# Optimization experiments

Hardware: AMD Instinct MI355X
Metric: run time of the kernel (lower is better)

Reference implementation:

```python
import jax, jax.numpy as jnp
import numpy as np

H = 128            # hidden_size; also the chunk length from torch.split(x, hidden_size)
NUM_CHUNKS = 4096  # B
INPUT_SIZE = 1
NUM_CLASSES = 1


def setup_inputs() -> dict:
    key = jax.random.key(0)
    ks = jax.random.split(key, 7)
    N = NUM_CHUNKS * H
    s = 1.0 / np.sqrt(H).astype(np.float32)
    x = jax.random.normal(ks[0], (N,), dtype=jnp.float32)
    W_ih = jax.random.uniform(ks[1], (4 * H, INPUT_SIZE), minval=-s, maxval=s, dtype=jnp.float32)
    W_hh = jax.random.uniform(ks[2], (4 * H, H), minval=-s, maxval=s, dtype=jnp.float32)
    b_ih = jax.random.uniform(ks[3], (4 * H,), minval=-s, maxval=s, dtype=jnp.float32)
    b_hh = jax.random.uniform(ks[4], (4 * H,), minval=-s, maxval=s, dtype=jnp.float32)
    fc_W = jax.random.uniform(ks[5], (NUM_CLASSES, H), minval=-s, maxval=s, dtype=jnp.float32)
    fc_b = jax.random.uniform(ks[6], (NUM_CLASSES,), minval=-s, maxval=s, dtype=jnp.float32)
    return {"x": x, "W_ih": W_ih, "W_hh": W_hh, "b_ih": b_ih, "b_hh": b_hh,
            "fc_W": fc_W, "fc_b": fc_b}


def reference(x, W_ih, W_hh, b_ih, b_hh, fc_W, fc_b):
    # Original: split flat x into chunks of length H, run each chunk as a
    # batch-1 LSTM (input_size=1), take final hidden state, apply fc_out.
    # Here all chunks are batched into one fused recurrent pass.
    Hh = W_hh.shape[1]
    xb = x.reshape(-1, Hh, 1)                                  # [B, T=H, 1]
    # input projection is time-parallel: precompute gate pre-activations
    pre = jnp.einsum('bti,gi->btg', xb, W_ih) + b_ih + b_hh    # [B, T, 4H]

    def step(carry, p_t):
        h, c = carry                                           # [B, H] each
        gates = p_t + h @ W_hh.T                               # [B, 4H]
        i, f, g, o = jnp.split(gates, 4, axis=-1)              # PyTorch gate order i,f,g,o
        i = jax.nn.sigmoid(i)
        f = jax.nn.sigmoid(f)
        g = jnp.tanh(g)
        o = jax.nn.sigmoid(o)
        c = f * c + i * g
        h = o * jnp.tanh(c)
        return (h, c), None

    B = xb.shape[0]
    h0 = jnp.zeros((B, Hh), dtype=x.dtype)
    c0 = jnp.zeros((B, Hh), dtype=x.dtype)
    (hT, _), _ = jax.lax.scan(step, (h0, c0), jnp.swapaxes(pre, 0, 1))
    return hT @ fc_W.T + fc_b                                  # [B, num_classes]
```

## Files before the change

### kernel.cpp

```cpp
#include <hip/hip_runtime.h>


#define H   128
#define T   128
#define MB  16
#define BLOCK 512
#define HSTRIDE 136

typedef _Float16 f16x8 __attribute__((ext_vector_type(8)));
typedef float    f32x4 __attribute__((ext_vector_type(4)));

__device__ __forceinline__ float fsig(float v) {
    float e = __expf(-v);
    return __builtin_amdgcn_rcpf(1.0f + e);
}
__device__ __forceinline__ float ftanh(float v) {
    float e = __expf(2.0f * v);
    return 1.0f - 2.0f * __builtin_amdgcn_rcpf(1.0f + e);
}

__launch_bounds__(BLOCK, 2)
__global__ void lstm_fused_kernel(const float* __restrict__ x,
                                  const float* __restrict__ W_ih,
                                  const float* __restrict__ W_hh,
                                  const float* __restrict__ b_ih,
                                  const float* __restrict__ b_hh,
                                  const float* __restrict__ fc_W,
                                  const float* __restrict__ fc_b,
                                  float* __restrict__ out)
{
    __shared__ float xs[MB][T];
    __shared__ __align__(16) _Float16 hbuf[2][MB][HSTRIDE];

    const int tid  = threadIdx.x;
    const int wave = tid >> 6;
    const int lane = tid & 63;
    const int l15  = lane & 15;
    const int q    = lane >> 4;
    const int jcol = wave * 16 + l15;

    {
        const float4* src = (const float4*)(x + (size_t)blockIdx.x * (MB * T));
        float4* dst = (float4*)(&xs[0][0]);
        dst[tid] = src[tid];
    }
    for (int i = tid; i < MB * HSTRIDE; i += BLOCK)
        (&hbuf[0][0][0])[i] = (_Float16)0.0f;

    f16x8 wf[4][4];
    float wih[4], bias[4];
    #pragma unroll
    for (int g = 0; g < 4; ++g) {
        const int n = g * H + jcol;
        wih[g]  = W_ih[n];
        bias[g] = b_ih[n] + b_hh[n];
        #pragma unroll
        for (int kc = 0; kc < 4; ++kc) {
            const float* wp = W_hh + (size_t)n * H + kc * 32 + q * 8;
            float4 w0 = ((const float4*)wp)[0];
            float4 w1 = ((const float4*)wp)[1];
            f16x8 f;
            f[0] = (_Float16)w0.x; f[1] = (_Float16)w0.y;
            f[2] = (_Float16)w0.z; f[3] = (_Float16)w0.w;
            f[4] = (_Float16)w1.x; f[5] = (_Float16)w1.y;
            f[6] = (_Float16)w1.z; f[7] = (_Float16)w1.w;
            wf[g][kc] = f;
        }
    }

    float c[4] = {0.f, 0.f, 0.f, 0.f};

    __syncthreads();

    for (int t = 0; t < T; ++t) {
        const int rb = t & 1;
        const int wb = rb ^ 1;

        f16x8 af[4];
        #pragma unroll
        for (int kc = 0; kc < 4; ++kc)
            af[kc] = *(const f16x8*)&hbuf[rb][l15][kc * 32 + q * 8];

        f32x4 acc[4];
        #pragma unroll
        for (int g = 0; g < 4; ++g) {
            #pragma unroll
            for (int r = 0; r < 4; ++r) {
                const int b = q * 4 + r;
                acc[g][r] = xs[b][t] * wih[g] + bias[g];
            }
        }

        #pragma unroll
        for (int kc = 0; kc < 4; ++kc) {
            #pragma unroll
            for (int g = 0; g < 4; ++g)
                acc[g] = __builtin_amdgcn_mfma_f32_16x16x32_f16(af[kc], wf[g][kc], acc[g], 0, 0, 0);
        }

        #pragma unroll
        for (int r = 0; r < 4; ++r) {
            const int b = q * 4 + r;
            float ig = fsig(acc[0][r]);
            float fg = fsig(acc[1][r]);
            float gg = ftanh(acc[2][r]);
            float og = fsig(acc[3][r]);
            float cn = fg * c[r] + ig * gg;
            c[r] = cn;
            float hv = og * ftanh(cn);
            hbuf[wb][b][jcol] = (_Float16)hv;
        }
        __syncthreads();
    }

    if (tid < 256) {
        const int b    = tid >> 4;
        const int part = tid & 15;
        const _Float16* hrow = &hbuf[0][b][0];
        float s = 0.0f;
        #pragma unroll
        for (int i = 0; i < 8; ++i) {
            const int j = part * 8 + i;
            s += fc_W[j] * (float)hrow[j];
        }
        s += __shfl_xor(s, 8, 16);
        s += __shfl_xor(s, 4, 16);
        s += __shfl_xor(s, 2, 16);
        s += __shfl_xor(s, 1, 16);
        if (part == 0)
            out[blockIdx.x * MB + b] = s + fc_b[0];
    }
}

extern "C" void kernel_launch(void* const* d_in, const int* in_sizes, int n_in,
                              void* d_out, int out_size, void* d_ws, size_t ws_size,
                              hipStream_t stream)
{
    const float* x    = (const float*)d_in[0];
    const float* W_ih = (const float*)d_in[1];
    const float* W_hh = (const float*)d_in[2];
    const float* b_ih = (const float*)d_in[3];
    const float* b_hh = (const float*)d_in[4];
    const float* fc_W = (const float*)d_in[5];
    const float* fc_b = (const float*)d_in[6];
    float* out = (float*)d_out;

    const int B = in_sizes[0] / H;
    dim3 grid(B / MB);
    dim3 block(BLOCK);
    hipLaunchKernelGGL(lstm_fused_kernel, grid, block, 0, stream,
                       x, W_ih, W_hh, b_ih, b_hh, fc_W, fc_b, out);
}
```

Baseline: 177.9 us.

## Prepack W_hh fragments, transpose x in LDS, merge gate reciprocals, prefetch input term

Adds a small prep kernel that converts W_hh to fp16 in MFMA fragment order in the workspace, so each block loads its weights with vector loads instead of converting them itself. x is stored time-major in LDS so the next step's input projection can be read with one float4 and computed ahead, and it is fed straight in as the MFMA accumulator init. The gate nonlinearities are rewritten algebraically so several sigmoid/tanh reciprocals share a single rcp per element, cutting transcendental work on the serial recurrence path. The cost is an extra kernel launch and some risk of overflow/NaN when the exp terms grow large.

```diff
diff --git a/kernel.cpp b/kernel.cpp
--- a/kernel.cpp
+++ b/kernel.cpp
@@ -6,30 +6,41 @@
 #define MB  16
 #define BLOCK 512
 #define HSTRIDE 136
+#define XSTRIDE 20
 
 typedef _Float16 f16x8 __attribute__((ext_vector_type(8)));
 typedef float    f32x4 __attribute__((ext_vector_type(4)));
 
-__device__ __forceinline__ float fsig(float v) {
-    float e = __expf(-v);
-    return __builtin_amdgcn_rcpf(1.0f + e);
+__global__ void prep_whh_kernel(const float* __restrict__ W_hh, _Float16* __restrict__ wfrag)
+{
+    int idx = blockIdx.x * blockDim.x + threadIdx.x;
+    int l15 =  idx        & 15;
+    int q   = (idx >> 4)  & 3;
+    int kc  = (idx >> 6)  & 3;
+    int g   = (idx >> 8)  & 3;
+    int ct  = (idx >> 10) & 7;
+    int n  = g * H + ct * 16 + l15;
+    int k0 = kc * 32 + q * 8;
+    const float* src = W_hh + (size_t)n * H + k0;
+    f16x8 f;
+    #pragma unroll
+    for (int i = 0; i < 8; ++i) f[i] = (_Float16)src[i];
+    *(f16x8*)(wfrag + (size_t)idx * 8) = f;
 }
-__device__ __forceinline__ float ftanh(float v) {
-    float e = __expf(2.0f * v);
-    return 1.0f - 2.0f * __builtin_amdgcn_rcpf(1.0f + e);
-}
+
+__device__ __forceinline__ float frcp(float v) { return __builtin_amdgcn_rcpf(v); }
 
 __launch_bounds__(BLOCK, 2)
 __global__ void lstm_fused_kernel(const float* __restrict__ x,
                                   const float* __restrict__ W_ih,
-                                  const float* __restrict__ W_hh,
+                                  const _Float16* __restrict__ wfrag,
                                   const float* __restrict__ b_ih,
                                   const float* __restrict__ b_hh,
                                   const float* __restrict__ fc_W,
                                   const float* __restrict__ fc_b,
                                   float* __restrict__ out)
 {
-    __shared__ float xs[MB][T];
+    __shared__ __align__(16) float xs[T + 1][XSTRIDE];
     __shared__ __align__(16) _Float16 hbuf[2][MB][HSTRIDE];
 
     const int tid  = threadIdx.x;
@@ -40,37 +51,54 @@
     const int jcol = wave * 16 + l15;
 
     {
-        const float4* src = (const float4*)(x + (size_t)blockIdx.x * (MB * T));
-        float4* dst = (float4*)(&xs[0][0]);
-        dst[tid] = src[tid];
+        const int t0 = tid & 127;
+        const int b0 = (tid >> 7) * 4;
+        const float* xb = x + (size_t)blockIdx.x * (MB * T);
+        #pragma unroll
+        for (int bb = 0; bb < 4; ++bb)
+            xs[t0][b0 + bb] = xb[(b0 + bb) * T + t0];
     }
     for (int i = tid; i < MB * HSTRIDE; i += BLOCK)
         (&hbuf[0][0][0])[i] = (_Float16)0.0f;
 
     f16x8 wf[4][4];
+    {
+        const _Float16* wbase = wfrag + (size_t)wave * (4 * 4 * 4 * 16 * 8);
+        #pragma unroll
+        for (int g = 0; g < 4; ++g)
+            #pragma unroll
+            for (int kc = 0; kc < 4; ++kc)
+                wf[g][kc] = *(const f16x8*)(wbase + ((((g * 4 + kc) * 4 + q) * 16 + l15) * 8));
+        #pragma unroll
+        for (int g = 0; g < 4; ++g)
+            #pragma unroll
+            for (int kc = 0; kc < 4; ++kc)
+                asm volatile("" : "+v"(wf[g][kc]));
+    }
+
     float wih[4], bias[4];
     #pragma unroll
     for (int g = 0; g < 4; ++g) {
         const int n = g * H + jcol;
         wih[g]  = W_ih[n];
         bias[g] = b_ih[n] + b_hh[n];
+    }
+
+    float c0[4] = {0.f, 0.f, 0.f, 0.f};
+
+    __syncthreads();
+
+    f32x4 initv[4];
+    {
+        float4 xl = *(const float4*)&xs[0][q * 4];
         #pragma unroll
-        for (int kc = 0; kc < 4; ++kc) {
-            const float* wp = W_hh + (size_t)n * H + kc * 32 + q * 8;
-            float4 w0 = ((const float4*)wp)[0];
-            float4 w1 = ((const float4*)wp)[1];
-            f16x8 f;
-            f[0] = (_Float16)w0.x; f[1] = (_Float16)w0.y;
-            f[2] = (_Float16)w0.z; f[3] = (_Float16)w0.w;
-            f[4] = (_Float16)w1.x; f[5] = (_Float16)w1.y;
-            f[6] = (_Float16)w1.z; f[7] = (_Float16)w1.w;
-            wf[g][kc] = f;
+        for (int g = 0; g < 4; ++g) {
+            initv[g][0] = fmaf(xl.x, wih[g], bias[g]);
+            initv[g][1] = fmaf(xl.y, wih[g], bias[g]);
+            initv[g][2] = fmaf(xl.z, wih[g], bias[g]);
+            initv[g][3] = fmaf(xl.w, wih[g], bias[g]);
         }
     }
-
-    float c[4] = {0.f, 0.f, 0.f, 0.f};
-
-    __syncthreads();
 
     for (int t = 0; t < T; ++t) {
         const int rb = t & 1;
@@ -83,31 +111,42 @@
 
         f32x4 acc[4];
         #pragma unroll
-        for (int g = 0; g < 4; ++g) {
-            #pragma unroll
-            for (int r = 0; r < 4; ++r) {
-                const int b = q * 4 + r;
-                acc[g][r] = xs[b][t] * wih[g] + bias[g];
-            }
-        }
-
+        for (int g = 0; g < 4; ++g)
+            acc[g] = __builtin_amdgcn_mfma_f32_16x16x32_f16(af[0], wf[g][0], initv[g], 0, 0, 0);
         #pragma unroll
-        for (int kc = 0; kc < 4; ++kc) {
+        for (int kc = 1; kc < 4; ++kc)
             #pragma unroll
             for (int g = 0; g < 4; ++g)
                 acc[g] = __builtin_amdgcn_mfma_f32_16x16x32_f16(af[kc], wf[g][kc], acc[g], 0, 0, 0);
+
+        {
+            float4 xl = *(const float4*)&xs[t + 1][q * 4];
+            #pragma unroll
+            for (int g = 0; g < 4; ++g) {
+                initv[g][0] = fmaf(xl.x, wih[g], bias[g]);
+                initv[g][1] = fmaf(xl.y, wih[g], bias[g]);
+                initv[g][2] = fmaf(xl.z, wih[g], bias[g]);
+                initv[g][3] = fmaf(xl.w, wih[g], bias[g]);
+            }
         }
 
         #pragma unroll
         for (int r = 0; r < 4; ++r) {
             const int b = q * 4 + r;
-            float ig = fsig(acc[0][r]);
-            float fg = fsig(acc[1][r]);
-            float gg = ftanh(acc[2][r]);
-            float og = fsig(acc[3][r]);
-            float cn = fg * c[r] + ig * gg;
-            c[r] = cn;
-            float hv = og * ftanh(cn);
+            float ai = acc[0][r], afv = acc[1][r], ag = acc[2][r], ao = acc[3][r];
+            float Ei = __expf(-ai);
+            float Ef = __expf(-afv);
+            float Eg = __expf(2.0f * ag);
+            float u  = 1.0f + Ei;
+            float v  = 1.0f + Ef;
+            float w  = 1.0f + Eg;
+            float wm = Eg - 1.0f;
+            float uw = u * w;
+            float cn = fmaf(c0[r], uw, wm * v) * frcp(v * uw);
+            c0[r] = cn;
+            float Eo = __expf(-ao);
+            float Ec = __expf(2.0f * cn);
+            float hv = (Ec - 1.0f) * frcp((Ec + 1.0f) * (1.0f + Eo));
             hbuf[wb][b][jcol] = (_Float16)hv;
         }
         __syncthreads();
@@ -145,9 +184,13 @@
     const float* fc_b = (const float*)d_in[6];
     float* out = (float*)d_out;
 
+    _Float16* wfrag = (_Float16*)d_ws;
+
+    hipLaunchKernelGGL(prep_whh_kernel, dim3(32), dim3(256), 0, stream, W_hh, wfrag);
+
     const int B = in_sizes[0] / H;
     dim3 grid(B / MB);
     dim3 block(BLOCK);
     hipLaunchKernelGGL(lstm_fused_kernel, grid, block, 0, stream,
-                       x, W_ih, W_hh, b_ih, b_hh, fc_W, fc_b, out);
+                       x, W_ih, wfrag, b_ih, b_hh, fc_W, fc_b, out);
 }
```

New measurement: 171.0 us. 3.9% less time.
